# Optimization experiments

Measured on AMD Instinct MI355X. Metric: run time of the kernel, lower is better.

The kernel has to match this reference:

```python
import jax, jax.numpy as jnp
import numpy as np

C = 343.0      # speed of sound (init kwarg c)
F = 16         # number of frequency channels (len(omega))
H = 128        # MLP hidden width
N = 131072     # collocation points


def _mlp(coords, W1, b1, W2, b2, W3, b3):
    # coords: [..., 3] -> [..., 2F] (first F = real part, last F = imag part)
    h = jnp.tanh(coords @ W1 + b1)
    h = jnp.tanh(h @ W2 + b2)
    return h @ W3 + b3


def setup_inputs() -> dict:
    key = jax.random.key(0)
    ks = jax.random.split(key, 4)
    inputs = jax.random.normal(ks[0], (N, 3), dtype=jnp.float32)
    # omega = 2*pi*f for f = 100..1600 Hz (matches init kwarg list)
    omega = 2.0 * jnp.pi * 100.0 * jnp.arange(1, F + 1, dtype=jnp.float32)
    s_in = 1.0 / np.sqrt(3.0)
    s_h = 1.0 / np.sqrt(float(H))
    W1 = jax.random.normal(ks[1], (3, H), dtype=jnp.float32) * s_in
    b1 = jnp.zeros((H,), dtype=jnp.float32)
    W2 = jax.random.normal(ks[2], (H, H), dtype=jnp.float32) * s_h
    b2 = jnp.zeros((H,), dtype=jnp.float32)
    W3 = jax.random.normal(ks[3], (H, 2 * F), dtype=jnp.float32) * s_h
    b3 = jnp.zeros((2 * F,), dtype=jnp.float32)
    return {"inputs": inputs, "omega": omega, "W1": W1, "b1": b1,
            "W2": W2, "b2": b2, "W3": W3, "b3": b3}


def reference(inputs, omega, W1, b1, W2, b2, W3, b3):
    # Pointwise network R^3 -> R^{2F} (real/imag stacked).
    f = lambda c3: _mlp(c3, W1, b1, W2, b2, W3, b3)

    # u: complex pressure per point per frequency, [N, F]
    out = _mlp(inputs, W1, b1, W2, b2, W3, b3)           # [N, 2F]
    u = out[:, :F] + 1j * out[:, F:]

    # Full spatial Hessian per point via forward-over-reverse AD (fused
    # replacement for the torch per-channel autograd.grad loop).
    hess = jax.vmap(jax.jacfwd(jax.jacrev(f)))(inputs)   # [N, 2F, 3, 3]
    lap_ri = jnp.einsum('nfii->nf', hess)                # diagonal trace = Laplacian
    lap = lap_ri[:, :F] + 1j * lap_ri[:, F:]             # [N, F] complex

    # PDE residual skips channel 0, exactly as the torch loop (i+1 indexing).
    k2 = (omega[1:] / C) ** 2                            # [F-1]
    residual = lap[:, 1:] + k2 * u[:, 1:]                # [N, F-1]

    # mean over channels then over batch == global mean of |residual|^2
    return jnp.mean(jnp.abs(residual) ** 2)
```

## Files before the change

kernel.cpp:

```cpp
#include <hip/hip_runtime.h>
#include <math.h>

#ifndef __has_builtin
#define __has_builtin(x) 0
#endif

#define NPTS   131072
#define FCH    16
#define CSND   343.0f
#define PB     16
#define BLOCK  256
#define GRID   512
#define NBLK   (NPTS / PB)

typedef _Float16 half8 __attribute__((ext_vector_type(8)));
typedef _Float16 half2v __attribute__((ext_vector_type(2)));
typedef float    f32x4 __attribute__((ext_vector_type(4)));

static __device__ __forceinline__ unsigned pack2(float a, float b) {
#if __has_builtin(__builtin_amdgcn_cvt_pkrtz)
  return __builtin_bit_cast(unsigned, __builtin_amdgcn_cvt_pkrtz(a, b));
#else
  half2v v; v[0] = (_Float16)a; v[1] = (_Float16)b;
  return __builtin_bit_cast(unsigned, v);
#endif
}

static __device__ __forceinline__ float mytanh(float x) {
#if __has_builtin(__builtin_amdgcn_exp2f)
  float e = __builtin_amdgcn_exp2f(2.885390082f * x);
#else
  float e = __expf(2.0f * x);
#endif
  return fmaf(-2.0f, __builtin_amdgcn_rcpf(e + 1.0f), 1.0f);
}


__global__ __launch_bounds__(BLOCK, 2) void helmholtz_kernel(
    const float* __restrict__ x,
    const float* __restrict__ omega,
    const float* __restrict__ W1,
    const float* __restrict__ b1,
    const float* __restrict__ W2,
    const float* __restrict__ b2,
    const float* __restrict__ W3,
    const float* __restrict__ b3,
    float* __restrict__ out)
{
  __shared__ unsigned s_A[2][80 * 64];
  __shared__ unsigned s_HG[2][32 * 64];

  const int tid  = threadIdx.x;
  const int w    = tid >> 6;
  const int l    = tid & 63;
  const int col  = l & 15;
  const int quad = l >> 4;

  const int pA = tid >> 4;
  const int g  = tid & 15;
  float wx[8], wy[8], wz[8], bB[8], wq[8];
#pragma unroll
  for (int u = 0; u < 8; u++) {
    int unit = 8 * g + u;
    wx[u] = W1[unit]; wy[u] = W1[128 + unit]; wz[u] = W1[256 + unit];
    bB[u] = b1[unit];
    wq[u] = wx[u] * wx[u] + wy[u] * wy[u] + wz[u] * wz[u];
  }

  half8 w2f[2][4];
#pragma unroll
  for (int ntl = 0; ntl < 2; ntl++) {
    const int n = (2 * w + ntl) * 16 + col;
#pragma unroll
    for (int ks = 0; ks < 4; ks++) {
      half8 f;
#pragma unroll
      for (int j = 0; j < 8; j++)
        f[j] = (_Float16)W2[(ks * 32 + (quad << 3) + j) * 128 + n];
      w2f[ntl][ks] = f;
    }
  }
  half8 w3f[4];
  {
    const int n = (w & 1) * 16 + col;
#pragma unroll
    for (int ks = 0; ks < 4; ks++) {
      half8 f;
#pragma unroll
      for (int j = 0; j < 8; j++)
        f[j] = (_Float16)W3[(ks * 32 + (quad << 3) + j) * 32 + n];
      w3f[ks] = f;
    }
  }

  const float b2r0 = b2[2 * w * 16 + col];
  const float b2r1 = b2[(2 * w + 1) * 16 + col];
  float k2v = 0.0f;
  if (col >= 1) {
    float om = omega[col] * (1.0f / CSND);
    k2v = om * om;
  }
  const float b3v = b3[(w & 1) * 16 + col];

  float wsum = 0.0f;

  auto phaseA = [&](int blk, int buf) {
    const float* xp = x + (size_t)(blk * PB + pA) * 3;
    float x0 = xp[0], x1 = xp[1], x2 = xp[2];
    float t[8], s[8];
#pragma unroll
    for (int u = 0; u < 8; u++) {
      float z = fmaf(x0, wx[u], fmaf(x1, wy[u], fmaf(x2, wz[u], bB[u])));
      t[u] = mytanh(z);
      s[u] = 1.0f - t[u] * t[u];
    }
    unsigned* sA = s_A[buf];
    const int base = (g ^ pA) << 2;
    uint4 q;
    q = make_uint4(pack2(t[0], t[1]), pack2(t[2], t[3]),
                   pack2(t[4], t[5]), pack2(t[6], t[7]));
    *(uint4*)&sA[(pA)      * 64 + base] = q;
    q = make_uint4(pack2(s[0] * wx[0], s[1] * wx[1]), pack2(s[2] * wx[2], s[3] * wx[3]),
                   pack2(s[4] * wx[4], s[5] * wx[5]), pack2(s[6] * wx[6], s[7] * wx[7]));
    *(uint4*)&sA[(16 + pA) * 64 + base] = q;
    q = make_uint4(pack2(s[0] * wy[0], s[1] * wy[1]), pack2(s[2] * wy[2], s[3] * wy[3]),
                   pack2(s[4] * wy[4], s[5] * wy[5]), pack2(s[6] * wy[6], s[7] * wy[7]));
    *(uint4*)&sA[(32 + pA) * 64 + base] = q;
    q = make_uint4(pack2(s[0] * wz[0], s[1] * wz[1]), pack2(s[2] * wz[2], s[3] * wz[3]),
                   pack2(s[4] * wz[4], s[5] * wz[5]), pack2(s[6] * wz[6], s[7] * wz[7]));
    *(uint4*)&sA[(48 + pA) * 64 + base] = q;
    float c[8];
#pragma unroll
    for (int u = 0; u < 8; u++) c[u] = -2.0f * t[u] * s[u] * wq[u];
    q = make_uint4(pack2(c[0], c[1]), pack2(c[2], c[3]),
                   pack2(c[4], c[5]), pack2(c[6], c[7]));
    *(uint4*)&sA[(64 + pA) * 64 + base] = q;
  };

  auto phaseDE = [&](int buf) {
    const unsigned* hgb = s_HG[buf];
    f32x4 dy = (f32x4){0.0f, 0.0f, 0.0f, 0.0f};
    f32x4 dl = (f32x4){0.0f, 0.0f, 0.0f, 0.0f};
#pragma unroll
    for (int ks = 0; ks < 4; ks++) {
      int ca = (ks * 4 + quad) ^ col;
      half8 afy = *(const half8*)&hgb[(col)      * 64 + (ca << 2)];
      half8 afl = *(const half8*)&hgb[(16 + col) * 64 + (ca << 2)];
      dy = __builtin_amdgcn_mfma_f32_16x16x32_f16(afy, w3f[ks], dy, 0, 0, 0);
      dl = __builtin_amdgcn_mfma_f32_16x16x32_f16(afl, w3f[ks], dl, 0, 0, 0);
    }
    if (col >= 1) {
#pragma unroll
      for (int r = 0; r < 4; r++) {
        float yv  = dy[r] + b3v;
        float res = fmaf(k2v, yv, dl[r]);
        wsum += res * res;
      }
    }
  };

  phaseA(blockIdx.x, 0);
  __syncthreads();

  int parity = 0;
  for (int blk = blockIdx.x; blk < NBLK; blk += gridDim.x, parity ^= 1) {
    if (w < 2 && blk != (int)blockIdx.x) phaseDE(parity ^ 1);

    int nblk = blk + (int)gridDim.x;
    if (nblk < NBLK) phaseA(nblk, parity ^ 1);

    const unsigned* sA = s_A[parity];
    f32x4 acc[5][2];
#pragma unroll
    for (int mt = 0; mt < 5; mt++)
#pragma unroll
      for (int ntl = 0; ntl < 2; ntl++)
        acc[mt][ntl] = (f32x4){0.0f, 0.0f, 0.0f, 0.0f};

#pragma unroll
    for (int mt = 0; mt < 5; mt++) {
      int m = mt * 16 + col;
#pragma unroll
      for (int ks = 0; ks < 4; ks++) {
        int c = (ks * 4 + quad) ^ col;
        half8 af = *(const half8*)&sA[m * 64 + (c << 2)];
        acc[mt][0] = __builtin_amdgcn_mfma_f32_16x16x32_f16(af, w2f[0][ks], acc[mt][0], 0, 0, 0);
        acc[mt][1] = __builtin_amdgcn_mfma_f32_16x16x32_f16(af, w2f[1][ks], acc[mt][1], 0, 0, 0);
      }
    }

    {
      _Float16* hg = (_Float16*)s_HG[parity];
#pragma unroll
      for (int ntl = 0; ntl < 2; ntl++) {
        int j = (2 * w + ntl) * 16 + col;
        int chunkj = j >> 3;
        float b2v = ntl ? b2r1 : b2r0;
#pragma unroll
        for (int r = 0; r < 4; r++) {
          int p = quad * 4 + r;
          float z2 = acc[0][ntl][r] + b2v;
          float d0 = acc[1][ntl][r], d1 = acc[2][ntl][r], d2 = acc[3][ntl][r];
          float Av = acc[4][ntl][r];
          float t2 = mytanh(z2);
          float s2 = 1.0f - t2 * t2;
          float gg = s2 * (Av - 2.0f * t2 * (d0 * d0 + d1 * d1 + d2 * d2));
          int base = ((chunkj ^ p) << 3) + (j & 7);
          hg[p * 128 + base]        = (_Float16)t2;
          hg[(16 + p) * 128 + base] = (_Float16)gg;
        }
      }
    }
    __syncthreads();
  }

  if (w < 2) phaseDE(parity ^ 1);

#pragma unroll
  for (int off = 32; off > 0; off >>= 1)
    wsum += __shfl_down(wsum, off, 64);
  if (l == 0)
    atomicAdd(out, wsum * (1.0f / ((float)NPTS * (float)(FCH - 1))));
}

extern "C" void kernel_launch(void* const* d_in, const int* in_sizes, int n_in,
                              void* d_out, int out_size, void* d_ws, size_t ws_size,
                              hipStream_t stream) {
  const float* x     = (const float*)d_in[0];
  const float* omega = (const float*)d_in[1];
  const float* W1    = (const float*)d_in[2];
  const float* b1    = (const float*)d_in[3];
  const float* W2    = (const float*)d_in[4];
  const float* b2    = (const float*)d_in[5];
  const float* W3    = (const float*)d_in[6];
  const float* b3    = (const float*)d_in[7];
  float* out = (float*)d_out;

  (void)hipMemsetAsync(out, 0, sizeof(float), stream);
  helmholtz_kernel<<<GRID, BLOCK, 0, stream>>>(x, omega, W1, b1, W2, b2, W3, b3, out);
}
```

Before: 121.4 us.

## Double points per block, widen MFMA N-tiles, drop LDS double buffering

Raises the points per block iteration from 16 to 32 and has each wave cover 16 points by 64 hidden units. Each A fragment loaded from LDS now feeds four MFMAs instead of two, and all four waves take part in the output layer. It drops the double-buffered LDS in favour of register prefetch of the next block's coordinates. W3 rows are permuted so the packed-pair layout of hidden outputs lines up with the MFMA K ordering, and hidden outputs are written as packed half2. This gives more data reuse and fewer blocks per CTA, at the cost of more accumulator registers and less overlap between phases.

```diff
diff --git a/kernel.cpp b/kernel.cpp
--- a/kernel.cpp
+++ b/kernel.cpp
@@ -8,7 +8,7 @@
 #define NPTS   131072
 #define FCH    16
 #define CSND   343.0f
-#define PB     16
+#define PB     32
 #define BLOCK  256
 #define GRID   512
 #define NBLK   (NPTS / PB)
@@ -47,14 +47,16 @@
     const float* __restrict__ b3,
     float* __restrict__ out)
 {
-  __shared__ unsigned s_A[2][80 * 64];
-  __shared__ unsigned s_HG[2][32 * 64];
+  __shared__ unsigned s_A[160 * 64];
+  __shared__ unsigned s_HG[32 * 128];
 
   const int tid  = threadIdx.x;
   const int w    = tid >> 6;
   const int l    = tid & 63;
   const int col  = l & 15;
   const int quad = l >> 4;
+  const int ph   = w >> 1;
+  const int nh   = w & 1;
 
   const int pA = tid >> 4;
   const int g  = tid & 15;
@@ -67,85 +69,99 @@
     wq[u] = wx[u] * wx[u] + wy[u] * wy[u] + wz[u] * wz[u];
   }
 
-  half8 w2f[2][4];
-#pragma unroll
-  for (int ntl = 0; ntl < 2; ntl++) {
-    const int n = (2 * w + ntl) * 16 + col;
+  half8 w2f[4][4];
+#pragma unroll
+  for (int t4 = 0; t4 < 4; t4++) {
+    const int n = 64 * nh + 16 * t4 + col;
 #pragma unroll
     for (int ks = 0; ks < 4; ks++) {
       half8 f;
 #pragma unroll
-      for (int j = 0; j < 8; j++)
-        f[j] = (_Float16)W2[(ks * 32 + (quad << 3) + j) * 128 + n];
-      w2f[ntl][ks] = f;
+      for (int j8 = 0; j8 < 8; j8++)
+        f[j8] = (_Float16)W2[(ks * 32 + (quad << 3) + j8) * 128 + n];
+      w2f[t4][ks] = f;
     }
   }
   half8 w3f[4];
-  {
-    const int n = (w & 1) * 16 + col;
-#pragma unroll
-    for (int ks = 0; ks < 4; ks++) {
-      half8 f;
-#pragma unroll
-      for (int j = 0; j < 8; j++)
-        f[j] = (_Float16)W3[(ks * 32 + (quad << 3) + j) * 32 + n];
-      w3f[ks] = f;
-    }
-  }
-
-  const float b2r0 = b2[2 * w * 16 + col];
-  const float b2r1 = b2[(2 * w + 1) * 16 + col];
+#pragma unroll
+  for (int ks = 0; ks < 4; ks++) {
+    half8 f;
+#pragma unroll
+    for (int j8 = 0; j8 < 8; j8++) {
+      int kap = ks * 32 + (quad << 3) + j8;
+      int q   = kap >> 1;
+      int j   = 64 * (q >> 5) + 32 * ((q >> 4) & 1) + 16 * (kap & 1) + (q & 15);
+      f[j8] = (_Float16)W3[j * 32 + 16 * nh + col];
+    }
+    w3f[ks] = f;
+  }
+
+  float b2r[4];
+#pragma unroll
+  for (int t4 = 0; t4 < 4; t4++) b2r[t4] = b2[64 * nh + 16 * t4 + col];
   float k2v = 0.0f;
   if (col >= 1) {
     float om = omega[col] * (1.0f / CSND);
     k2v = om * om;
   }
-  const float b3v = b3[(w & 1) * 16 + col];
+  const float b3v = b3[16 * nh + col];
 
   float wsum = 0.0f;
-
-  auto phaseA = [&](int blk, int buf) {
-    const float* xp = x + (size_t)(blk * PB + pA) * 3;
-    float x0 = xp[0], x1 = xp[1], x2 = xp[2];
-    float t[8], s[8];
-#pragma unroll
-    for (int u = 0; u < 8; u++) {
-      float z = fmaf(x0, wx[u], fmaf(x1, wy[u], fmaf(x2, wz[u], bB[u])));
-      t[u] = mytanh(z);
-      s[u] = 1.0f - t[u] * t[u];
-    }
-    unsigned* sA = s_A[buf];
-    const int base = (g ^ pA) << 2;
-    uint4 q;
-    q = make_uint4(pack2(t[0], t[1]), pack2(t[2], t[3]),
-                   pack2(t[4], t[5]), pack2(t[6], t[7]));
-    *(uint4*)&sA[(pA)      * 64 + base] = q;
-    q = make_uint4(pack2(s[0] * wx[0], s[1] * wx[1]), pack2(s[2] * wx[2], s[3] * wx[3]),
-                   pack2(s[4] * wx[4], s[5] * wx[5]), pack2(s[6] * wx[6], s[7] * wx[7]));
-    *(uint4*)&sA[(16 + pA) * 64 + base] = q;
-    q = make_uint4(pack2(s[0] * wy[0], s[1] * wy[1]), pack2(s[2] * wy[2], s[3] * wy[3]),
-                   pack2(s[4] * wy[4], s[5] * wy[5]), pack2(s[6] * wy[6], s[7] * wy[7]));
-    *(uint4*)&sA[(32 + pA) * 64 + base] = q;
-    q = make_uint4(pack2(s[0] * wz[0], s[1] * wz[1]), pack2(s[2] * wz[2], s[3] * wz[3]),
-                   pack2(s[4] * wz[4], s[5] * wz[5]), pack2(s[6] * wz[6], s[7] * wz[7]));
-    *(uint4*)&sA[(48 + pA) * 64 + base] = q;
-    float c[8];
-#pragma unroll
-    for (int u = 0; u < 8; u++) c[u] = -2.0f * t[u] * s[u] * wq[u];
-    q = make_uint4(pack2(c[0], c[1]), pack2(c[2], c[3]),
-                   pack2(c[4], c[5]), pack2(c[6], c[7]));
-    *(uint4*)&sA[(64 + pA) * 64 + base] = q;
+  float xr[2][3];
+
+  auto loadX = [&](int blk) {
+    const float* xb = x + (size_t)blk * PB * 3;
+#pragma unroll
+    for (int hp = 0; hp < 2; hp++) {
+      int p = pA + 16 * hp;
+      xr[hp][0] = xb[3 * p]; xr[hp][1] = xb[3 * p + 1]; xr[hp][2] = xb[3 * p + 2];
+    }
   };
 
-  auto phaseDE = [&](int buf) {
-    const unsigned* hgb = s_HG[buf];
+  auto phaseA = [&]() {
+    const int cbase = (g ^ pA) << 2;
+#pragma unroll
+    for (int hp = 0; hp < 2; hp++) {
+      int p = pA + 16 * hp;
+      float x0 = xr[hp][0], x1 = xr[hp][1], x2 = xr[hp][2];
+      float t[8], s[8];
+#pragma unroll
+      for (int u = 0; u < 8; u++) {
+        float z = fmaf(x0, wx[u], fmaf(x1, wy[u], fmaf(x2, wz[u], bB[u])));
+        t[u] = mytanh(z);
+        s[u] = 1.0f - t[u] * t[u];
+      }
+      uint4 q;
+      q = make_uint4(pack2(t[0], t[1]), pack2(t[2], t[3]),
+                     pack2(t[4], t[5]), pack2(t[6], t[7]));
+      *(uint4*)&s_A[(p)       * 64 + cbase] = q;
+      q = make_uint4(pack2(s[0]*wx[0], s[1]*wx[1]), pack2(s[2]*wx[2], s[3]*wx[3]),
+                     pack2(s[4]*wx[4], s[5]*wx[5]), pack2(s[6]*wx[6], s[7]*wx[7]));
+      *(uint4*)&s_A[(32 + p)  * 64 + cbase] = q;
+      q = make_uint4(pack2(s[0]*wy[0], s[1]*wy[1]), pack2(s[2]*wy[2], s[3]*wy[3]),
+                     pack2(s[4]*wy[4], s[5]*wy[5]), pack2(s[6]*wy[6], s[7]*wy[7]));
+      *(uint4*)&s_A[(64 + p)  * 64 + cbase] = q;
+      q = make_uint4(pack2(s[0]*wz[0], s[1]*wz[1]), pack2(s[2]*wz[2], s[3]*wz[3]),
+                     pack2(s[4]*wz[4], s[5]*wz[5]), pack2(s[6]*wz[6], s[7]*wz[7]));
+      *(uint4*)&s_A[(96 + p)  * 64 + cbase] = q;
+      float c[8];
+#pragma unroll
+      for (int u = 0; u < 8; u++) c[u] = -2.0f * t[u] * s[u] * wq[u];
+      q = make_uint4(pack2(c[0], c[1]), pack2(c[2], c[3]),
+                     pack2(c[4], c[5]), pack2(c[6], c[7]));
+      *(uint4*)&s_A[(128 + p) * 64 + cbase] = q;
+    }
+  };
+
+  auto phaseDE = [&]() {
+    const int pbase = (16 * ph + col) * 128;
     f32x4 dy = (f32x4){0.0f, 0.0f, 0.0f, 0.0f};
     f32x4 dl = (f32x4){0.0f, 0.0f, 0.0f, 0.0f};
 #pragma unroll
     for (int ks = 0; ks < 4; ks++) {
-      int ca = (ks * 4 + quad) ^ col;
-      half8 afy = *(const half8*)&hgb[(col)      * 64 + (ca << 2)];
-      half8 afl = *(const half8*)&hgb[(16 + col) * 64 + (ca << 2)];
+      int pos = ((((ks << 2) + quad) ^ col) << 2);
+      half8 afy = *(const half8*)&s_HG[pbase + pos];
+      half8 afl = *(const half8*)&s_HG[pbase + 64 + pos];
       dy = __builtin_amdgcn_mfma_f32_16x16x32_f16(afy, w3f[ks], dy, 0, 0, 0);
       dl = __builtin_amdgcn_mfma_f32_16x16x32_f16(afl, w3f[ks], dl, 0, 0, 0);
     }
@@ -159,62 +175,63 @@
     }
   };
 
-  phaseA(blockIdx.x, 0);
-  __syncthreads();
-
-  int parity = 0;
-  for (int blk = blockIdx.x; blk < NBLK; blk += gridDim.x, parity ^= 1) {
-    if (w < 2 && blk != (int)blockIdx.x) phaseDE(parity ^ 1);
+  loadX(blockIdx.x);
+  bool first = true;
+  for (int blk = blockIdx.x; blk < NBLK; blk += gridDim.x) {
+    if (!first) phaseDE();
+    first = false;
+    phaseA();
+    __syncthreads();
 
     int nblk = blk + (int)gridDim.x;
-    if (nblk < NBLK) phaseA(nblk, parity ^ 1);
-
-    const unsigned* sA = s_A[parity];
-    f32x4 acc[5][2];
-#pragma unroll
-    for (int mt = 0; mt < 5; mt++)
-#pragma unroll
-      for (int ntl = 0; ntl < 2; ntl++)
-        acc[mt][ntl] = (f32x4){0.0f, 0.0f, 0.0f, 0.0f};
-
-#pragma unroll
-    for (int mt = 0; mt < 5; mt++) {
-      int m = mt * 16 + col;
+    if (nblk < NBLK) loadX(nblk);
+
+    f32x4 acc[5][4];
+#pragma unroll
+    for (int v = 0; v < 5; v++)
+#pragma unroll
+      for (int t4 = 0; t4 < 4; t4++)
+        acc[v][t4] = (f32x4){0.0f, 0.0f, 0.0f, 0.0f};
+
+#pragma unroll
+    for (int v = 0; v < 5; v++) {
+      const int rb = (v * 32 + 16 * ph + col) * 64;
 #pragma unroll
       for (int ks = 0; ks < 4; ks++) {
-        int c = (ks * 4 + quad) ^ col;
-        half8 af = *(const half8*)&sA[m * 64 + (c << 2)];
-        acc[mt][0] = __builtin_amdgcn_mfma_f32_16x16x32_f16(af, w2f[0][ks], acc[mt][0], 0, 0, 0);
-        acc[mt][1] = __builtin_amdgcn_mfma_f32_16x16x32_f16(af, w2f[1][ks], acc[mt][1], 0, 0, 0);
-      }
-    }
-
-    {
-      _Float16* hg = (_Float16*)s_HG[parity];
-#pragma unroll
-      for (int ntl = 0; ntl < 2; ntl++) {
-        int j = (2 * w + ntl) * 16 + col;
-        int chunkj = j >> 3;
-        float b2v = ntl ? b2r1 : b2r0;
-#pragma unroll
-        for (int r = 0; r < 4; r++) {
-          int p = quad * 4 + r;
-          float z2 = acc[0][ntl][r] + b2v;
-          float d0 = acc[1][ntl][r], d1 = acc[2][ntl][r], d2 = acc[3][ntl][r];
-          float Av = acc[4][ntl][r];
-          float t2 = mytanh(z2);
-          float s2 = 1.0f - t2 * t2;
-          float gg = s2 * (Av - 2.0f * t2 * (d0 * d0 + d1 * d1 + d2 * d2));
-          int base = ((chunkj ^ p) << 3) + (j & 7);
-          hg[p * 128 + base]        = (_Float16)t2;
-          hg[(16 + p) * 128 + base] = (_Float16)gg;
-        }
+        half8 af = *(const half8*)&s_A[rb + ((((ks << 2) + quad) ^ col) << 2)];
+        acc[v][0] = __builtin_amdgcn_mfma_f32_16x16x32_f16(af, w2f[0][ks], acc[v][0], 0, 0, 0);
+        acc[v][1] = __builtin_amdgcn_mfma_f32_16x16x32_f16(af, w2f[1][ks], acc[v][1], 0, 0, 0);
+        acc[v][2] = __builtin_amdgcn_mfma_f32_16x16x32_f16(af, w2f[2][ks], acc[v][2], 0, 0, 0);
+        acc[v][3] = __builtin_amdgcn_mfma_f32_16x16x32_f16(af, w2f[3][ks], acc[v][3], 0, 0, 0);
+      }
+    }
+
+#pragma unroll
+    for (int r = 0; r < 4; r++) {
+      int p = 16 * ph + (quad << 2) + r;
+      float t2[4], gg[4];
+#pragma unroll
+      for (int t4 = 0; t4 < 4; t4++) {
+        float z2 = acc[0][t4][r] + b2r[t4];
+        float d0 = acc[1][t4][r], d1 = acc[2][t4][r], d2 = acc[3][t4][r];
+        float Av = acc[4][t4][r];
+        float t  = mytanh(z2);
+        float s2 = 1.0f - t * t;
+        t2[t4] = t;
+        gg[t4] = s2 * (Av - 2.0f * t * (d0 * d0 + d1 * d1 + d2 * d2));
+      }
+      int pb = p * 128;
+#pragma unroll
+      for (int pr = 0; pr < 2; pr++) {
+        int q   = 32 * nh + 16 * pr + col;
+        int pos = (((q >> 2) ^ (p & 15)) << 2) + (q & 3);
+        s_HG[pb + pos]      = pack2(t2[2 * pr], t2[2 * pr + 1]);
+        s_HG[pb + 64 + pos] = pack2(gg[2 * pr], gg[2 * pr + 1]);
       }
     }
     __syncthreads();
   }
-
-  if (w < 2) phaseDE(parity ^ 1);
+  phaseDE();
 
 #pragma unroll
   for (int off = 32; off > 0; off >>= 1)
```

New measurement: 124.4 us. +2.5%, slower.
